# Optimization experiments

Hardware: AMD Instinct MI355X
Metric: run time of the kernel (lower is better)

Reference implementation:

```python
import jax, jax.numpy as jnp
import numpy as np
import math

B, L, S, D = 4, 4096, 4096, 256
EPS = 1e-5

def _layernorm(x, g, b):
    mu = jnp.mean(x, axis=-1, keepdims=True)
    var = jnp.mean(jnp.square(x - mu), axis=-1, keepdims=True)
    return (x - mu) * jax.lax.rsqrt(var + EPS) * g + b

def setup_inputs() -> dict:
    key = jax.random.key(0)
    ks = jax.random.split(key, 14)
    s = 1.0 / math.sqrt(D)
    s2 = 1.0 / math.sqrt(2 * D)
    inp = {
        "source": jax.random.normal(ks[0], (B, L, D), jnp.float32),
        "target": jax.random.normal(ks[1], (B, S, D), jnp.float32),
        # linear weights stored as [in, out]
        "Wq": jax.random.uniform(ks[2], (D, D), jnp.float32, -s, s),
        "bq": jnp.zeros((D,), jnp.float32),
        "Wk": jax.random.uniform(ks[3], (D, D), jnp.float32, -s, s),
        "bk": jnp.zeros((D,), jnp.float32),
        "Wv": jax.random.uniform(ks[4], (D, D), jnp.float32, -s, s),
        "bv": jnp.zeros((D,), jnp.float32),
        "Wm": jax.random.uniform(ks[5], (D, D), jnp.float32, -s, s),
        "bm": jnp.zeros((D,), jnp.float32),
        "g1": jnp.ones((D,), jnp.float32),
        "beta1": jnp.zeros((D,), jnp.float32),
        "W1": jax.random.uniform(ks[6], (2 * D, 2 * D), jnp.float32, -s2, s2),
        "W2": jax.random.uniform(ks[7], (2 * D, D), jnp.float32, -s2, s2),
        "g2": jnp.ones((D,), jnp.float32),
        "beta2": jnp.zeros((D,), jnp.float32),
    }
    return inp

def reference(source, target, Wq, bq, Wk, bk, Wv, bv, Wm, bm, g1, beta1, W1, W2, g2, beta2):
    q = source @ Wq + bq              # [B, L, D]
    k = target @ Wk + bk              # [B, S, D]
    v = target @ Wv + bv              # [B, S, D]
    scale = 1.0 / math.sqrt(D)
    scores = jnp.einsum("bld,bsd->bls", q, k) * scale   # [B, L, S] materialized, as in source
    attn = jax.nn.softmax(scores, axis=-1)
    message = jnp.einsum("bls,bsd->bld", attn, v)        # [B, L, D]
    message = message @ Wm + bm
    message = _layernorm(message, g1, beta1)
    h = jnp.concatenate([source, message], axis=-1)      # [B, L, 2D]
    h = jax.nn.gelu(h @ W1, approximate=False)           # torch GELU is exact erf
    message = _layernorm(h @ W2, g2, beta2)
    return source + message
```

## Files before the change

kernel.cpp:

```cpp
#include <hip/hip_runtime.h>

typedef __bf16 bf16x8 __attribute__((ext_vector_type(8)));
typedef float f32x16 __attribute__((ext_vector_type(16)));
typedef float f32x4 __attribute__((ext_vector_type(4)));
typedef unsigned int u32;
typedef unsigned int u32x4 __attribute__((ext_vector_type(4)));
typedef unsigned short u16;
typedef unsigned short u16x4 __attribute__((ext_vector_type(4)));
typedef unsigned short u16x8 __attribute__((ext_vector_type(8)));

#define DEV static __device__ __forceinline__
#define AS1 __attribute__((address_space(1)))
#define AS3 __attribute__((address_space(3)))

DEV u16 f2bf(float f){
  unsigned u = __float_as_uint(f);
  u += 0x7FFFu + ((u >> 16) & 1u);
  return (u16)(u >> 16);
}
DEV float bf2f(u16 h){ return __uint_as_float(((u32)h) << 16); }

DEV void stage16(const u16* gsrc, const u16* ldst){
  __builtin_amdgcn_global_load_lds((const AS1 u32*)(unsigned long long)gsrc,
                                   (AS3 u32*)(u32)(unsigned long long)ldst,
                                   16, 0, 0);
}

constexpr int BATCH = 4, LQ = 4096, SK = 4096, DH = 256, BL = BATCH * LQ;
constexpr int NHALF = 2;
constexpr int ITERS = SK / NHALF / 64;

__global__ void prep_weights(const float* __restrict__ Wq, const float* __restrict__ Wk,
                             const float* __restrict__ Wv, const float* __restrict__ Wm,
                             const float* __restrict__ W1, const float* __restrict__ W2,
                             const float* __restrict__ bk, const float* __restrict__ bv,
                             u16* __restrict__ WqT, u16* __restrict__ WkvT,
                             u16* __restrict__ WmT,
                             u16* __restrict__ W1T, u16* __restrict__ W2T,
                             float* __restrict__ bkv){
  int idx = blockIdx.x * 256 + threadIdx.x;
  if (idx < 262144){
    int which = idx >> 16, i2 = idx & 65535;
    int r = i2 >> 8, c = i2 & 255;
    const float* S = (which==0)?Wq:(which==1)?Wk:(which==2)?Wv:Wm;
    u16*         D = (which==0)?WqT:(which==1)?WkvT:(which==2)?(WkvT+65536):WmT;
    D[c*256 + r] = f2bf(S[i2]);
  } else if (idx < 524288){
    int i2 = idx - 262144;
    int r = i2 >> 9, c = i2 & 511;
    W1T[c*512 + r] = f2bf(W1[i2]);
  } else if (idx < 655360){
    int i2 = idx - 524288;
    int r = i2 >> 8, c = i2 & 255;
    W2T[(size_t)c*512 + r] = f2bf(W2[i2]);
  } else if (idx < 655872){
    int i2 = idx - 655360;
    bkv[i2] = (i2 < 256) ? bk[i2] : bv[i2 - 256];
  }
}

__global__ __launch_bounds__(512, 2) void qkv_gemm(
  const float* __restrict__ src, const float* __restrict__ tgt,
  const u16* __restrict__ WqT, const u16* __restrict__ WkvT,
  const float* __restrict__ bq, const float* __restrict__ bkv,
  u16* __restrict__ qbuf, u16* __restrict__ kbuf, u16* __restrict__ vtbuf,
  float qscale)
{
  __shared__ u16 A_lds[64 * 64];
  __shared__ u16 B_lds[256 * 64];
  const int tid = threadIdx.x, lane = tid & 63, wid = tid >> 6;
  const int ql = lane & 31, g = lane >> 5;
  const int path = blockIdx.x;
  const int m0 = blockIdx.y * 64;
  const float* Af = (path == 0) ? src : tgt;
  const u16* BTp = (path == 0) ? WqT : (WkvT + (size_t)(path - 1) * 65536);
  const float* bias = (path == 0) ? bq : (bkv + (path - 1) * 256);
  const int ar = tid >> 3, ac = (tid & 7) * 8;

  f32x16 acc[2] = {};
  f32x4 af0, af1;
  u32x4 breg[4];

#define QKV_LOAD_A(kb) do { \
    af0 = *(const f32x4*)&Af[(size_t)(m0+ar)*256 + (kb)*64 + ac]; \
    af1 = *(const f32x4*)&Af[(size_t)(m0+ar)*256 + (kb)*64 + ac + 4]; \
  } while(0)
#define QKV_LOAD_B(kb) do { \
    _Pragma("unroll") \
    for (int i = 0; i < 4; i++){ int item = tid + i*512; int r = item>>3, c = (item&7)*8; \
      breg[i] = *(const u32x4*)&BTp[(size_t)r*256 + (kb)*64 + c]; } \
  } while(0)

  QKV_LOAD_A(0); QKV_LOAD_B(0);

  for (int kb = 0; kb < 4; ++kb){
    __syncthreads();
    { u16x8 h;
      h[0]=f2bf(af0[0]); h[1]=f2bf(af0[1]); h[2]=f2bf(af0[2]); h[3]=f2bf(af0[3]);
      h[4]=f2bf(af1[0]); h[5]=f2bf(af1[1]); h[6]=f2bf(af1[2]); h[7]=f2bf(af1[3]);
      *(u16x8*)&A_lds[ar*64 + (ac ^ ((ar&7)*8))] = h;
    }
    #pragma unroll
    for (int i = 0; i < 4; i++){ int item = tid + i*512; int r = item>>3, c = (item&7)*8;
      *(u32x4*)&B_lds[r*64 + (c ^ ((r&7)*8))] = breg[i]; }
    __syncthreads();
    if (kb + 1 < 4){ QKV_LOAD_A(kb+1); QKV_LOAD_B(kb+1); }

    #pragma unroll
    for (int kk = 0; kk < 4; kk++){
      bf16x8 af[2];
      #pragma unroll
      for (int mi = 0; mi < 2; mi++)
        af[mi] = __builtin_bit_cast(bf16x8,
          *(const u32x4*)&A_lds[(mi*32+ql)*64 + ((kk*16+g*8) ^ ((ql&7)*8))]);
      bf16x8 bf = __builtin_bit_cast(bf16x8,
        *(const u32x4*)&B_lds[(wid*32+ql)*64 + ((kk*16+g*8) ^ ((ql&7)*8))]);
      #pragma unroll
      for (int mi = 0; mi < 2; mi++)
        acc[mi] = __builtin_amdgcn_mfma_f32_32x32x16_bf16(af[mi], bf, acc[mi], 0, 0, 0);
    }
  }

  const int col = wid*32 + ql;
  const float bv = bias[col];
  if (path == 2){
    #pragma unroll
    for (int mi = 0; mi < 2; mi++)
      #pragma unroll
      for (int qd = 0; qd < 4; qd++){
        u16x4 h;
        #pragma unroll
        for (int i = 0; i < 4; i++) h[i] = f2bf(acc[mi][qd*4+i] + bv);
        int row0 = m0 + mi*32 + qd*8 + 4*g;
        int bb = row0 >> 12, ss = row0 & 4095;
        *(u16x4*)&vtbuf[((size_t)bb*DH + col)*SK + ss] = h;
      }
  } else {
    u16* outp = (path == 0) ? qbuf : kbuf;
    const float sc = (path == 0) ? qscale : 1.0f;
    #pragma unroll
    for (int mi = 0; mi < 2; mi++)
      #pragma unroll
      for (int j = 0; j < 16; j++){
        int row = m0 + mi*32 + (j&3) + 8*(j>>2) + 4*g;
        outp[(size_t)row*256 + col] = f2bf((acc[mi][j] + bv) * sc);
      }
  }
}

__global__ __launch_bounds__(512, 2) void wm_mlp(
  const u16* __restrict__ opart, const float* __restrict__ stats,
  const u16* __restrict__ WmT, const float* __restrict__ bm,
  const float* __restrict__ g1, const float* __restrict__ be1,
  const u16* __restrict__ W1T, const u16* __restrict__ W2T,
  const float* __restrict__ g2, const float* __restrict__ be2,
  const float* __restrict__ src, float* __restrict__ outp)
{
  __shared__ __align__(16) char smem[131328];
  u16* Hc = (u16*)smem;
  char* rb = smem + 65536;
  u16* A_lds = (u16*)rb;
  u16* B_lds = (u16*)(rb + 8192);
  float* scr = (float*)rb;
  u16* B1 = (u16*)rb;
  u16* B2 = (u16*)rb;

  const int tid = threadIdx.x, lane = tid & 63, wid = tid >> 6;
  const int ql = lane & 31, g = lane >> 5;
  const int m0 = blockIdx.x * 64;
  const int ar = tid >> 3, ac = (tid & 7) * 8;

  #pragma unroll
  for (int i = 0; i < 4; i++){
    int idx = tid + i*512;
    int r = idx >> 5, c8 = (idx & 31) * 8;
    f32x4 a = *(const f32x4*)&src[(size_t)(m0+r)*256 + c8];
    f32x4 b = *(const f32x4*)&src[(size_t)(m0+r)*256 + c8 + 4];
    u16x8 h;
    h[0]=f2bf(a[0]); h[1]=f2bf(a[1]); h[2]=f2bf(a[2]); h[3]=f2bf(a[3]);
    h[4]=f2bf(b[0]); h[5]=f2bf(b[1]); h[6]=f2bf(b[2]); h[7]=f2bf(b[3]);
    int s = c8 >> 3;
    *(u16x8*)&Hc[r*512 + ((s ^ (r&7))<<3)] = h;
  }

  float winv;
  { int row = m0 + ar;
    winv = 1.f / (stats[row] + stats[(size_t)BL + row]); }

  f32x16 acc[2] = {};
  u32x4 areg, areg2;
  u32x4 breg[4];

#define WM_LOAD_A(kb) do { \
    areg  = *(const u32x4*)&opart[(size_t)(m0+ar)*DH + (kb)*64 + ac]; \
    areg2 = *(const u32x4*)&opart[(size_t)BL*DH + (size_t)(m0+ar)*DH + (kb)*64 + ac]; \
  } while(0)
#define WM_LOAD_B(kb) do { \
    _Pragma("unroll") \
    for (int i = 0; i < 4; i++){ int item = tid + i*512; int r = item>>3, c = (item&7)*8; \
      breg[i] = *(const u32x4*)&BTpWm[(size_t)r*256 + (kb)*64 + c]; } \
  } while(0)

  const u16* BTpWm = WmT;
  WM_LOAD_A(0); WM_LOAD_B(0);

  for (int kb = 0; kb < 4; ++kb){
    __syncthreads();
    { u16x8 h;
      #pragma unroll
      for (int e = 0; e < 8; e++){
        u16 h0 = (u16)(areg[e>>1]  >> ((e&1)*16));
        u16 h1 = (u16)(areg2[e>>1] >> ((e&1)*16));
        h[e] = f2bf((bf2f(h0) + bf2f(h1)) * winv);
      }
      *(u16x8*)&A_lds[ar*64 + (ac ^ ((ar&7)*8))] = h; }
    #pragma unroll
    for (int i = 0; i < 4; i++){ int item = tid + i*512; int r = item>>3, c = (item&7)*8;
      *(u32x4*)&B_lds[r*64 + (c ^ ((r&7)*8))] = breg[i]; }
    __syncthreads();
    if (kb + 1 < 4){ WM_LOAD_A(kb+1); WM_LOAD_B(kb+1); }

    #pragma unroll
    for (int kk = 0; kk < 4; kk++){
      bf16x8 af[2];
      #pragma unroll
      for (int mi = 0; mi < 2; mi++)
        af[mi] = __builtin_bit_cast(bf16x8,
          *(const u32x4*)&A_lds[(mi*32+ql)*64 + ((kk*16+g*8) ^ ((ql&7)*8))]);
      bf16x8 bf = __builtin_bit_cast(bf16x8,
        *(const u32x4*)&B_lds[(wid*32+ql)*64 + ((kk*16+g*8) ^ ((ql&7)*8))]);
      #pragma unroll
      for (int mi = 0; mi < 2; mi++)
        acc[mi] = __builtin_amdgcn_mfma_f32_32x32x16_bf16(af[mi], bf, acc[mi], 0, 0, 0);
    }
  }

  __syncthreads();

  { const float bv = bm[wid*32 + ql];
    #pragma unroll
    for (int mi = 0; mi < 2; mi++)
      #pragma unroll
      for (int j = 0; j < 16; j++){
        int row = mi*32 + (j&3) + 8*(j>>2) + 4*g;
        scr[row*257 + wid*32 + ql] = acc[mi][j] + bv;
      }
  }
  __syncthreads();

  { f32x4 gv = *(const f32x4*)&g1[lane*4];
    f32x4 bvv = *(const f32x4*)&be1[lane*4];
    #pragma unroll
    for (int rr = 0; rr < 8; rr++){
      const int row = wid*8 + rr;
      f32x4 v = *(const f32x4*)&scr[row*257 + lane*4];
      float s1 = v[0]+v[1]+v[2]+v[3];
      float s2 = v[0]*v[0]+v[1]*v[1]+v[2]*v[2]+v[3]*v[3];
      #pragma unroll
      for (int m = 1; m < 64; m <<= 1){ s1 += __shfl_xor(s1, m, 64); s2 += __shfl_xor(s2, m, 64); }
      float mu = s1 * (1.f/DH);
      float var = s2 * (1.f/DH) - mu*mu;
      float rstd = rsqrtf(var + 1e-5f);
      u16x4 h;
      #pragma unroll
      for (int i = 0; i < 4; i++) h[i] = f2bf((v[i]-mu)*rstd*gv[i] + bvv[i]);
      const int col = 256 + lane*4;
      const int s = col >> 3;
      *(u16x4*)&Hc[row*512 + ((s ^ (row&7))<<3) + (col & 7)] = h;
    }
  }
  __syncthreads();

  f32x16 acc1[2][2] = {};
  for (int kb = 0; kb < 8; ++kb){
    if (kb) __syncthreads();
    #pragma unroll
    for (int i = 0; i < 8; i++){
      int grp = tid + i*512; int r = grp>>3, slot = grp&7;
      stage16(&W1T[(size_t)r*512 + kb*64 + ((slot ^ (r&7))<<3)], &B1[grp*8]);
    }
    __syncthreads();
    #pragma unroll
    for (int kk = 0; kk < 4; kk++){
      const int c0s = (kb*64 + kk*16 + g*8) >> 3;
      bf16x8 af[2];
      #pragma unroll
      for (int mi = 0; mi < 2; mi++){
        int row = mi*32 + ql;
        af[mi] = __builtin_bit_cast(bf16x8,
          *(const u32x4*)&Hc[row*512 + ((c0s ^ (row&7))<<3)]);
      }
      #pragma unroll
      for (int ni = 0; ni < 2; ni++){
        int rB = wid*64 + ni*32 + ql;
        bf16x8 bf = __builtin_bit_cast(bf16x8,
          *(const u32x4*)&B1[rB*64 + ((kk*16+g*8) ^ ((ql&7)*8))]);
        #pragma unroll
        for (int mi = 0; mi < 2; mi++)
          acc1[mi][ni] = __builtin_amdgcn_mfma_f32_32x32x16_bf16(af[mi], bf, acc1[mi][ni], 0, 0, 0);
      }
    }
  }
  __syncthreads();

  #pragma unroll
  for (int mi = 0; mi < 2; mi++)
    #pragma unroll
    for (int ni = 0; ni < 2; ni++){
      const int col = wid*64 + ni*32 + ql;
      const int s = col >> 3;
      #pragma unroll
      for (int j = 0; j < 16; j++){
        int row = mi*32 + (j&3) + 8*(j>>2) + 4*g;
        float v = acc1[mi][ni][j];
        v = 0.5f * v * (1.f + erff(v * 0.70710678118f));
        Hc[row*512 + ((s ^ (row&7))<<3) + (col&7)] = f2bf(v);
      }
    }
  __syncthreads();

  f32x16 acc2[2] = {};
  for (int kb = 0; kb < 8; ++kb){
    if (kb) __syncthreads();
    #pragma unroll
    for (int i = 0; i < 4; i++){
      int grp = tid + i*512; int r = grp>>3, slot = grp&7;
      stage16(&W2T[(size_t)r*512 + kb*64 + ((slot ^ (r&7))<<3)], &B2[grp*8]);
    }
    __syncthreads();
    #pragma unroll
    for (int kk = 0; kk < 4; kk++){
      const int c0s = (kb*64 + kk*16 + g*8) >> 3;
      bf16x8 af[2];
      #pragma unroll
      for (int mi = 0; mi < 2; mi++){
        int row = mi*32 + ql;
        af[mi] = __builtin_bit_cast(bf16x8,
          *(const u32x4*)&Hc[row*512 + ((c0s ^ (row&7))<<3)]);
      }
      bf16x8 bf = __builtin_bit_cast(bf16x8,
        *(const u32x4*)&B2[(wid*32+ql)*64 + ((kk*16+g*8) ^ ((ql&7)*8))]);
      #pragma unroll
      for (int mi = 0; mi < 2; mi++)
        acc2[mi] = __builtin_amdgcn_mfma_f32_32x32x16_bf16(af[mi], bf, acc2[mi], 0, 0, 0);
    }
  }
  __syncthreads();

  #pragma unroll
  for (int mi = 0; mi < 2; mi++)
    #pragma unroll
    for (int j = 0; j < 16; j++){
      int row = mi*32 + (j&3) + 8*(j>>2) + 4*g;
      scr[row*257 + wid*32 + ql] = acc2[mi][j];
    }
  __syncthreads();

  { f32x4 gv = *(const f32x4*)&g2[lane*4];
    f32x4 bvv = *(const f32x4*)&be2[lane*4];
    #pragma unroll
    for (int rr = 0; rr < 8; rr++){
      const int row = wid*8 + rr;
      f32x4 v = *(const f32x4*)&scr[row*257 + lane*4];
      float s1 = v[0]+v[1]+v[2]+v[3];
      float s2 = v[0]*v[0]+v[1]*v[1]+v[2]*v[2]+v[3]*v[3];
      #pragma unroll
      for (int m = 1; m < 64; m <<= 1){ s1 += __shfl_xor(s1, m, 64); s2 += __shfl_xor(s2, m, 64); }
      float mu = s1 * (1.f/DH);
      float var = s2 * (1.f/DH) - mu*mu;
      float rstd = rsqrtf(var + 1e-5f);
      f32x4 s = *(const f32x4*)&src[(size_t)(m0+row)*DH + lane*4];
      f32x4 o;
      #pragma unroll
      for (int i = 0; i < 4; i++) o[i] = s[i] + (v[i]-mu)*rstd*gv[i] + bvv[i];
      *(f32x4*)&outp[(size_t)(m0+row)*DH + lane*4] = o;
    }
  }
}

__global__ __launch_bounds__(512, 2) void attn_kernel(
  const u16* __restrict__ qb, const u16* __restrict__ kb,
  const u16* __restrict__ vtb, u16* __restrict__ opart, float* __restrict__ stats)
{
  __shared__ u16 K_lds[2][64 * 256];
  __shared__ u16 VT_lds[2][256 * 64];
  __shared__ u32x4 P_exch[4][4][64];
  __shared__ float L_exch[4][2][32];

  const int tid = threadIdx.x;
  const int wid = tid >> 6, lane = tid & 63;
  const int ql = lane & 31, g = lane >> 5;
  const int qpair = wid >> 1, sh = wid & 1;
  const int b = blockIdx.y, half = blockIdx.z;
  const int qrow0 = blockIdx.x * 128 + qpair * 32;
  const int s0base = half * (SK / NHALF);

  const u16* kbase = kb  + (size_t)b * SK * DH;
  const u16* vbase = vtb + (size_t)b * DH * SK;

#define STAGE_K(bi, s0) do { \
    _Pragma("unroll") \
    for (int i = 0; i < 4; i++){ \
      int grp = tid + i*512; int s = grp>>5, slot = grp&31; \
      stage16(kbase + (size_t)((s0)+s)*DH + ((slot ^ (s&31))<<3), \
              &K_lds[bi][(i*512 + wid*64)*8]); \
    } } while(0)
#define STAGE_V(bi, s0) do { \
    _Pragma("unroll") \
    for (int i = 0; i < 4; i++){ \
      int grp = tid + i*512; int d = grp>>3, slot = grp&7; \
      stage16(vbase + (size_t)d*SK + (s0) + ((slot ^ (d&7))<<3), \
              &VT_lds[bi][(i*512 + wid*64)*8]); \
    } } while(0)

  STAGE_K(0, s0base);
  STAGE_V(0, s0base);

  bf16x8 qf[16];
  {
    const u16* qp = qb + ((size_t)(b*LQ + qrow0 + ql)) * DH + g * 8;
    #pragma unroll
    for (int kk = 0; kk < 16; kk++)
      qf[kk] = __builtin_bit_cast(bf16x8, *(const u32x4*)(qp + kk*16));
  }

  f32x16 accO[4] = {};
  float l_lane = 0.f;

  __syncthreads();

  for (int it = 0; it < ITERS; ++it){
    const int cur = it & 1;
    if (it + 1 < ITERS){
      STAGE_K(cur ^ 1, s0base + (it+1)*64);
      STAGE_V(cur ^ 1, s0base + (it+1)*64);
    }

    f32x16 ps = {};
    __builtin_amdgcn_s_setprio(1);
    #pragma unroll
    for (int kk = 0; kk < 16; ++kk){
      bf16x8 kf = __builtin_bit_cast(bf16x8,
        *(const u32x4*)&K_lds[cur][(sh*32+ql)*256 + (((kk*2+g) ^ ql)<<3)]);
      ps = __builtin_amdgcn_mfma_f32_32x32x16_bf16(kf, qf[kk], ps, 0, 0, 0);
    }
    __builtin_amdgcn_s_setprio(0);

    #pragma unroll
    for (int j = 0; j < 16; j++) ps[j] = exp2f(ps[j]);

    u32 Wp[4][2];
    #pragma unroll
    for (int qd = 0; qd < 4; qd++)
      #pragma unroll
      for (int h = 0; h < 2; h++){
        float lo = ps[qd*4 + 2*h], hi = ps[qd*4 + 2*h + 1];
        asm("v_cvt_pk_bf16_f32 %0, %1, %2" : "=v"(Wp[qd][h]) : "v"(lo), "v"(hi));
      }
    bf16x8 pfo[2];
    #pragma unroll
    for (int i = 0; i < 2; i++){
      const int qp2 = i * 2;
      u32 a0 = Wp[qp2][0], b0 = Wp[qp2+1][0];
      u32 a1 = Wp[qp2][1], b1 = Wp[qp2+1][1];
      asm("v_permlane32_swap_b32 %0, %1" : "+v"(a0), "+v"(b0));
      asm("v_permlane32_swap_b32 %0, %1" : "+v"(a1), "+v"(b1));
      u32x4 w; w[0] = a0; w[1] = a1; w[2] = b0; w[3] = b1;
      P_exch[qpair][sh*2 + i][lane] = w;
      pfo[i] = __builtin_bit_cast(bf16x8, w);
    }

    __builtin_amdgcn_s_setprio(1);
    #pragma unroll
    for (int dt = 0; dt < 4; dt++){
      const int dtg = sh*4 + dt;
      const int k0 = sh*2;
      bf16x8 vf0 = __builtin_bit_cast(bf16x8,
        *(const u32x4*)&VT_lds[cur][(dtg*32+ql)*64 + ((((k0+0)*2+g) ^ (ql&7))<<3)]);
      accO[dt] = __builtin_amdgcn_mfma_f32_32x32x16_bf16(vf0, pfo[0], accO[dt], 0, 0, 0);
      bf16x8 vf1 = __builtin_bit_cast(bf16x8,
        *(const u32x4*)&VT_lds[cur][(dtg*32+ql)*64 + ((((k0+1)*2+g) ^ (ql&7))<<3)]);
      accO[dt] = __builtin_amdgcn_mfma_f32_32x32x16_bf16(vf1, pfo[1], accO[dt], 0, 0, 0);
    }
    __builtin_amdgcn_s_setprio(0);

    { float s8[8];
      #pragma unroll
      for (int j = 0; j < 8; j++) s8[j] = ps[j] + ps[j+8];
      l_lane += ((s8[0]+s8[4]) + (s8[1]+s8[5])) + ((s8[2]+s8[6]) + (s8[3]+s8[7])); }

    asm volatile("s_waitcnt lgkmcnt(0)" ::: "memory");
    __builtin_amdgcn_s_barrier();
    __builtin_amdgcn_sched_barrier(0);

    bf16x8 pfp0 = __builtin_bit_cast(bf16x8, P_exch[qpair][(sh^1)*2 + 0][lane]);
    bf16x8 pfp1 = __builtin_bit_cast(bf16x8, P_exch[qpair][(sh^1)*2 + 1][lane]);

    __builtin_amdgcn_s_setprio(1);
    #pragma unroll
    for (int dt = 0; dt < 4; dt++){
      const int dtg = sh*4 + dt;
      const int k0 = (sh^1)*2;
      bf16x8 vf0 = __builtin_bit_cast(bf16x8,
        *(const u32x4*)&VT_lds[cur][(dtg*32+ql)*64 + ((((k0+0)*2+g) ^ (ql&7))<<3)]);
      accO[dt] = __builtin_amdgcn_mfma_f32_32x32x16_bf16(vf0, pfp0, accO[dt], 0, 0, 0);
      bf16x8 vf1 = __builtin_bit_cast(bf16x8,
        *(const u32x4*)&VT_lds[cur][(dtg*32+ql)*64 + ((((k0+1)*2+g) ^ (ql&7))<<3)]);
      accO[dt] = __builtin_amdgcn_mfma_f32_32x32x16_bf16(vf1, pfp1, accO[dt], 0, 0, 0);
    }
    __builtin_amdgcn_s_setprio(0);

    asm volatile("s_waitcnt vmcnt(0) lgkmcnt(0)" ::: "memory");
    __builtin_amdgcn_s_barrier();
    __builtin_amdgcn_sched_barrier(0);
  }

  float l_run = l_lane + __shfl_xor(l_lane, 32, 64);
  if (g == 0) L_exch[qpair][sh][ql] = l_run;
  __syncthreads();
  float l_tot = l_run + L_exch[qpair][sh^1][ql];

  const int rowb = b * LQ + qrow0;
  if (sh == 0 && g == 0)
    stats[(size_t)half*BL + rowb + ql] = l_tot;

  float* scratch = (float*)&K_lds[0][0] + wid * 1056;
  #pragma unroll
  for (int dt = 0; dt < 4; dt++){
    const int dtg = sh*4 + dt;
    #pragma unroll
    for (int j = 0; j < 16; j++){
      int dl = (j&3) + 8*(j>>2) + 4*g;
      scratch[ql*33 + dl] = accO[dt][j];
    }
    int q2 = lane >> 1, dl2 = (lane & 1) * 16;
    u16x8 h0, h1;
    #pragma unroll
    for (int i = 0; i < 8; i++){ h0[i] = f2bf(scratch[q2*33 + dl2 + i]);
                                 h1[i] = f2bf(scratch[q2*33 + dl2 + 8 + i]); }
    u16* op = &opart[((size_t)half*BL + rowb + q2)*DH + dtg*32 + dl2];
    *(u16x8*)op = h0;
    *(u16x8*)(op + 8) = h1;
  }
}

extern "C" void kernel_launch(void* const* d_in, const int* in_sizes, int n_in,
                              void* d_out, int out_size, void* d_ws, size_t ws_size,
                              hipStream_t stream)
{
  const float* source = (const float*)d_in[0];
  const float* target = (const float*)d_in[1];
  const float* Wq = (const float*)d_in[2];  const float* bq = (const float*)d_in[3];
  const float* Wk = (const float*)d_in[4];  const float* bk = (const float*)d_in[5];
  const float* Wv = (const float*)d_in[6];  const float* bv = (const float*)d_in[7];
  const float* Wm = (const float*)d_in[8];  const float* bm = (const float*)d_in[9];
  const float* g1 = (const float*)d_in[10]; const float* be1 = (const float*)d_in[11];
  const float* W1 = (const float*)d_in[12]; const float* W2 = (const float*)d_in[13];
  const float* g2 = (const float*)d_in[14]; const float* be2 = (const float*)d_in[15];

  char* ws = (char*)d_ws;
  u16* WqT  = (u16*)(ws);
  u16* WkvT = (u16*)(ws + (size_t)(1u<<17));
  u16* WmT  = (u16*)(ws + (size_t)3*(1u<<17));
  u16* W1T  = (u16*)(ws + (size_t)4*(1u<<17));
  u16* W2T  = (u16*)(ws + (size_t)8*(1u<<17));
  float* bkv = (float*)(ws + (size_t)10*(1u<<17));
  size_t off = (size_t)10*(1u<<17) + 4096;
  u16* qbuf  = (u16*)(ws + off); off += (size_t)BL*DH*2;
  u16* kbuf  = (u16*)(ws + off); off += (size_t)BL*DH*2;
  u16* vtbuf = (u16*)(ws + off); off += (size_t)BL*DH*2;
  u16* opart = (u16*)(ws + off); off += (size_t)NHALF*BL*DH*2;
  float* stats = (float*)(ws + off); off += (size_t)NHALF*BL*4;

  prep_weights<<<dim3(2562), 256, 0, stream>>>(Wq, Wk, Wv, Wm, W1, W2, bk, bv,
                                               WqT, WkvT, WmT, W1T, W2T, bkv);

  const float qscale = 1.4426950408889634f / 16.0f;
  qkv_gemm<<<dim3(3, BL/64), 512, 0, stream>>>(
      source, target, WqT, WkvT, bq, bkv, qbuf, kbuf, vtbuf, qscale);

  attn_kernel<<<dim3(LQ/128, BATCH, NHALF), 512, 0, stream>>>(qbuf, kbuf, vtbuf, opart, stats);

  wm_mlp<<<dim3(BL/64), 512, 0, stream>>>(opart, stats, WmT, bm, g1, be1,
                                          W1T, W2T, g2, be2, source,
                                          (float*)d_out);
}
```

Before: 151.6 us.

## Shrink attention blocks to 256 threads with single-buffered K/V staging

Halves the attention block to 4 waves covering 64 query rows and drops the double-buffered K/V LDS tiles in favour of a single buffer. LDS per block shrinks from about 136KB to about 68KB, so more blocks can be resident per CU while the grid doubles. The cost is that global-to-LDS staging of the next tile no longer overlaps compute: it waits behind an extra barrier each iteration, and each K/V tile is now loaded by twice as many blocks.

```diff
diff --git a/kernel.cpp b/kernel.cpp
--- a/kernel.cpp
+++ b/kernel.cpp
@@ -378,43 +378,43 @@
   }
 }
 
-__global__ __launch_bounds__(512, 2) void attn_kernel(
+__global__ __launch_bounds__(256, 2) void attn_kernel(
   const u16* __restrict__ qb, const u16* __restrict__ kb,
   const u16* __restrict__ vtb, u16* __restrict__ opart, float* __restrict__ stats)
 {
-  __shared__ u16 K_lds[2][64 * 256];
-  __shared__ u16 VT_lds[2][256 * 64];
-  __shared__ u32x4 P_exch[4][4][64];
-  __shared__ float L_exch[4][2][32];
+  __shared__ u16 K_lds[64 * 256];
+  __shared__ u16 VT_lds[256 * 64];
+  __shared__ u32x4 P_exch[2][4][64];
+  __shared__ float L_exch[2][2][32];
 
   const int tid = threadIdx.x;
   const int wid = tid >> 6, lane = tid & 63;
   const int ql = lane & 31, g = lane >> 5;
   const int qpair = wid >> 1, sh = wid & 1;
   const int b = blockIdx.y, half = blockIdx.z;
-  const int qrow0 = blockIdx.x * 128 + qpair * 32;
+  const int qrow0 = blockIdx.x * 64 + qpair * 32;
   const int s0base = half * (SK / NHALF);
 
   const u16* kbase = kb  + (size_t)b * SK * DH;
   const u16* vbase = vtb + (size_t)b * DH * SK;
 
-#define STAGE_K(bi, s0) do { \
+#define STAGE_K(s0) do { \
     _Pragma("unroll") \
-    for (int i = 0; i < 4; i++){ \
-      int grp = tid + i*512; int s = grp>>5, slot = grp&31; \
+    for (int i = 0; i < 8; i++){ \
+      int grp = tid + i*256; int s = grp>>5, slot = grp&31; \
       stage16(kbase + (size_t)((s0)+s)*DH + ((slot ^ (s&31))<<3), \
-              &K_lds[bi][(i*512 + wid*64)*8]); \
+              &K_lds[(i*256 + wid*64)*8]); \
     } } while(0)
-#define STAGE_V(bi, s0) do { \
+#define STAGE_V(s0) do { \
     _Pragma("unroll") \
-    for (int i = 0; i < 4; i++){ \
-      int grp = tid + i*512; int d = grp>>3, slot = grp&7; \
+    for (int i = 0; i < 8; i++){ \
+      int grp = tid + i*256; int d = grp>>3, slot = grp&7; \
       stage16(vbase + (size_t)d*SK + (s0) + ((slot ^ (d&7))<<3), \
-              &VT_lds[bi][(i*512 + wid*64)*8]); \
+              &VT_lds[(i*256 + wid*64)*8]); \
     } } while(0)
 
-  STAGE_K(0, s0base);
-  STAGE_V(0, s0base);
+  STAGE_K(s0base);
+  STAGE_V(s0base);
 
   bf16x8 qf[16];
   {
@@ -430,18 +430,12 @@
   __syncthreads();
 
   for (int it = 0; it < ITERS; ++it){
-    const int cur = it & 1;
-    if (it + 1 < ITERS){
-      STAGE_K(cur ^ 1, s0base + (it+1)*64);
-      STAGE_V(cur ^ 1, s0base + (it+1)*64);
-    }
-
     f32x16 ps = {};
     __builtin_amdgcn_s_setprio(1);
     #pragma unroll
     for (int kk = 0; kk < 16; ++kk){
       bf16x8 kf = __builtin_bit_cast(bf16x8,
-        *(const u32x4*)&K_lds[cur][(sh*32+ql)*256 + (((kk*2+g) ^ ql)<<3)]);
+        *(const u32x4*)&K_lds[(sh*32+ql)*256 + (((kk*2+g) ^ ql)<<3)]);
       ps = __builtin_amdgcn_mfma_f32_32x32x16_bf16(kf, qf[kk], ps, 0, 0, 0);
     }
     __builtin_amdgcn_s_setprio(0);
@@ -476,10 +470,10 @@
       const int dtg = sh*4 + dt;
       const int k0 = sh*2;
       bf16x8 vf0 = __builtin_bit_cast(bf16x8,
-        *(const u32x4*)&VT_lds[cur][(dtg*32+ql)*64 + ((((k0+0)*2+g) ^ (ql&7))<<3)]);
+        *(const u32x4*)&VT_lds[(dtg*32+ql)*64 + ((((k0+0)*2+g) ^ (ql&7))<<3)]);
       accO[dt] = __builtin_amdgcn_mfma_f32_32x32x16_bf16(vf0, pfo[0], accO[dt], 0, 0, 0);
       bf16x8 vf1 = __builtin_bit_cast(bf16x8,
-        *(const u32x4*)&VT_lds[cur][(dtg*32+ql)*64 + ((((k0+1)*2+g) ^ (ql&7))<<3)]);
+        *(const u32x4*)&VT_lds[(dtg*32+ql)*64 + ((((k0+1)*2+g) ^ (ql&7))<<3)]);
       accO[dt] = __builtin_amdgcn_mfma_f32_32x32x16_bf16(vf1, pfo[1], accO[dt], 0, 0, 0);
     }
     __builtin_amdgcn_s_setprio(0);
@@ -502,15 +496,24 @@
       const int dtg = sh*4 + dt;
       const int k0 = (sh^1)*2;
       bf16x8 vf0 = __builtin_bit_cast(bf16x8,
-        *(const u32x4*)&VT_lds[cur][(dtg*32+ql)*64 + ((((k0+0)*2+g) ^ (ql&7))<<3)]);
+        *(const u32x4*)&VT_lds[(dtg*32+ql)*64 + ((((k0+0)*2+g) ^ (ql&7))<<3)]);
       accO[dt] = __builtin_amdgcn_mfma_f32_32x32x16_bf16(vf0, pfp0, accO[dt], 0, 0, 0);
       bf16x8 vf1 = __builtin_bit_cast(bf16x8,
-        *(const u32x4*)&VT_lds[cur][(dtg*32+ql)*64 + ((((k0+1)*2+g) ^ (ql&7))<<3)]);
+        *(const u32x4*)&VT_lds[(dtg*32+ql)*64 + ((((k0+1)*2+g) ^ (ql&7))<<3)]);
       accO[dt] = __builtin_amdgcn_mfma_f32_32x32x16_bf16(vf1, pfp1, accO[dt], 0, 0, 0);
     }
     __builtin_amdgcn_s_setprio(0);
 
-    asm volatile("s_waitcnt vmcnt(0) lgkmcnt(0)" ::: "memory");
+    asm volatile("s_waitcnt lgkmcnt(0)" ::: "memory");
+    __builtin_amdgcn_s_barrier();
+    __builtin_amdgcn_sched_barrier(0);
+
+    if (it + 1 < ITERS){
+      STAGE_K(s0base + (it+1)*64);
+      STAGE_V(s0base + (it+1)*64);
+    }
+
+    asm volatile("s_waitcnt vmcnt(0)" ::: "memory");
     __builtin_amdgcn_s_barrier();
     __builtin_amdgcn_sched_barrier(0);
   }
@@ -524,7 +527,7 @@
   if (sh == 0 && g == 0)
     stats[(size_t)half*BL + rowb + ql] = l_tot;
 
-  float* scratch = (float*)&K_lds[0][0] + wid * 1056;
+  float* scratch = (float*)&K_lds[0] + wid * 1056;
   #pragma unroll
   for (int dt = 0; dt < 4; dt++){
     const int dtg = sh*4 + dt;
@@ -579,7 +582,7 @@
   qkv_gemm<<<dim3(3, BL/64), 512, 0, stream>>>(
       source, target, WqT, WkvT, bq, bkv, qbuf, kbuf, vtbuf, qscale);
 
-  attn_kernel<<<dim3(LQ/128, BATCH, NHALF), 512, 0, stream>>>(qbuf, kbuf, vtbuf, opart, stats);
+  attn_kernel<<<dim3(LQ/64, BATCH, NHALF), 256, 0, stream>>>(qbuf, kbuf, vtbuf, opart, stats);
 
   wm_mlp<<<dim3(BL/64), 512, 0, stream>>>(opart, stats, WmT, bm, g1, be1,
                                           W1T, W2T, g2, be2, source,
```

Measured after the change: 165.6 us. 1.09x slower.
